# Kernel tuning notes

Hardware: AMD Instinct MI355X
Metric: run time of the kernel (lower is better)

Reference implementation:

```python
import jax, jax.numpy as jnp
import numpy as np

N = 50000      # nodes
E = 400000     # edges (avg degree 8)
N_IN = 256     # n_in_chan
N_HID = 256    # n_hid_chan


def gcn_conv(x, src, dst, W, b, n):
    """PyG GCNConv: D^{-1/2}(A+I)D^{-1/2} X W^T + b (add_self_loops=True, unit weights)."""
    h = x @ W.T                                           # [n, out]
    # degree over A + I: each node has a self loop (the initial ones) plus in-edges
    deg = jnp.ones((n,), h.dtype).at[dst].add(1.0)        # [n]
    dinv = jax.lax.rsqrt(deg)                             # deg >= 1 always
    norm = dinv[src] * dinv[dst]                          # [E]
    agg = jnp.zeros_like(h).at[dst].add(h[src] * norm[:, None])
    agg = agg + h * (dinv * dinv)[:, None]                # self-loop term, norm = dinv_i^2
    return agg + b


def setup_inputs() -> dict:
    key = jax.random.key(0)
    k1, k2, k3, k4 = jax.random.split(key, 4)
    x = jax.random.normal(k1, (N, N_IN + N_HID), dtype=jnp.float32)
    edge_index = jax.random.randint(k2, (2, E), 0, N, dtype=jnp.int64)
    s1 = 1.0 / np.sqrt(N_IN + N_HID)
    s2 = 1.0 / np.sqrt(N_HID)
    W1 = jax.random.normal(k3, (N_HID, N_IN + N_HID), dtype=jnp.float32) * s1
    W2 = jax.random.normal(k4, (N_HID, N_HID), dtype=jnp.float32) * s2
    b1 = jnp.zeros((N_HID,), jnp.float32)
    b2 = jnp.zeros((N_HID,), jnp.float32)
    return {"x": x, "edge_index": edge_index, "W1": W1, "b1": b1, "W2": W2, "b2": b2}


def reference(x, edge_index, W1, b1, W2, b2):
    src, dst = edge_index[0], edge_index[1]
    h = jax.nn.relu(gcn_conv(x, src, dst, W1, b1, N))
    return gcn_conv(h, src, dst, W2, b2, N)
```

## Files before the change

kernel.cpp:

```cpp
#include <hip/hip_runtime.h>
#include <hip/hip_bf16.h>

#define NN 50000
#define CH 256
#define SLOTS 96
#define G1K 512
#define G2K 256

typedef unsigned short u16;
typedef unsigned int   u32;

using short8 = __attribute__((ext_vector_type(8))) short;
using u16x8  = __attribute__((ext_vector_type(8))) unsigned short;
using f32x4  = __attribute__((ext_vector_type(4))) float;

static __device__ __forceinline__ float4 ld4(const float* p){ return *(const float4*)p; }

static __device__ __forceinline__ u16 f2b(float f){
  u32 u = __float_as_uint(f);
  u = (u + 0x7fffu + ((u >> 16) & 1u)) >> 16;
  return (u16)u;
}
static __device__ __forceinline__ float b2f(u16 b){
  return __uint_as_float(((u32)b) << 16);
}
static __device__ __forceinline__ int pkbf(float lo, float hi){
  __hip_bfloat162 h = __float22bfloat162_rn(make_float2(lo, hi));
  int r; __builtin_memcpy(&r, &h, 4); return r;
}

static __device__ __forceinline__ void gload_lds16(const void* g, void* l){
  __builtin_amdgcn_global_load_lds((const __attribute__((address_space(1))) void*)g,
                                   (__attribute__((address_space(3))) void*)l, 16, 0, 0);
}

#define WBAR(vm) do{ \
    asm volatile("s_waitcnt vmcnt(" #vm ") lgkmcnt(0)" ::: "memory"); \
    __builtin_amdgcn_s_barrier(); \
  }while(0)


__global__ void ell_build_kernel(const int* __restrict__ src, const int* __restrict__ dst,
                                 int* __restrict__ deg, int* __restrict__ ell, int E,
                                 const float* __restrict__ W1, u16* __restrict__ W1bf, int w1n4,
                                 const float* __restrict__ W2, u16* __restrict__ W2bf, int w2n4){
  int T = gridDim.x * 256;
  int g = blockIdx.x*256 + threadIdx.x;
  if (g < E){
    int d = dst[g];
    int pos = atomicAdd(&deg[d], 1);
    if (pos < SLOTS) ell[(size_t)d*SLOTS + pos] = src[g];
  }
  for (int i = g; i < w1n4; i += T){
    float4 v = ld4(W1 + (size_t)i*4);
    int2 o = { pkbf(v.x,v.y), pkbf(v.z,v.w) };
    *(int2*)(W1bf + (size_t)i*4) = o;
  }
  for (int i = g; i < w2n4; i += T){
    float4 v = ld4(W2 + (size_t)i*4);
    int2 o = { pkbf(v.x,v.y), pkbf(v.z,v.w) };
    *(int2*)(W2bf + (size_t)i*4) = o;
  }
}

__global__ void dinv_kernel(const int* __restrict__ deg, float* __restrict__ dinv, int n){
  int i = blockIdx.x*256 + threadIdx.x;
  if (i < n) dinv[i] = rsqrtf(1.0f + (float)deg[i]);
}


#define G1_GLB_B(kt, bb) do{ \
    gload_lds16(gB + (size_t)(kt)*32,          &Bs[bb][wave*2048]); \
    gload_lds16(gB + (size_t)(kt)*32 + 16*G1K, &Bs[bb][wave*2048 + 512]); \
    gload_lds16(gB + (size_t)(kt)*32 + 32*G1K, &Bs[bb][wave*2048 + 1024]); \
    gload_lds16(gB + (size_t)(kt)*32 + 48*G1K, &Bs[bb][wave*2048 + 1536]); \
  }while(0)

#define G1_GLB_A(kt, ab) do{ \
    gload_lds16(gA0 + (size_t)(kt)*32, &Asf[ab][wave*512]); \
    gload_lds16(gA1 + (size_t)(kt)*32, &Asf[ab][wave*512 + 256]); \
  }while(0)

#define G1_COMP(ra, rb) do{ \
    short8 af[4], bq[4]; \
    _Pragma("unroll") \
    for (int i=0;i<4;i++){ \
      int r = i*16 + lm; \
      float4 f0 = *(const float4*)&Asf[ra][r*32 + ((s0 ^ (lm&7))<<2)]; \
      float4 f1 = *(const float4*)&Asf[ra][r*32 + ((s1 ^ (lm&7))<<2)]; \
      int4 p = { pkbf(f0.x,f0.y), pkbf(f0.z,f0.w), pkbf(f1.x,f1.y), pkbf(f1.z,f1.w) }; \
      af[i] = *(short8*)&p; \
    } \
    _Pragma("unroll") \
    for (int j=0;j<4;j++) bq[j] = *(const short8*)&Bs[rb][(wave*64 + j*16 + lm)*32 + lk]; \
    _Pragma("unroll") \
    for (int i=0;i<4;i++) \
      _Pragma("unroll") \
      for (int j=0;j<4;j++) \
        acc[i][j] = __builtin_amdgcn_mfma_f32_16x16x32_bf16(af[i], bq[j], acc[i][j], 0, 0, 0); \
  }while(0)

__global__ __launch_bounds__(256, 2) void gemm1_kernel(const float* __restrict__ A,
                                                       const u16* __restrict__ Bbf,
                                                       u16* __restrict__ C, int M){
  __shared__ float Asf[3][64*32];
  __shared__ u16   Bs[2][256*32];
  int tid = threadIdx.x;
  int wave = tid >> 6, lane = tid & 63;
  int bm = blockIdx.x;

  int cslot = (lane & 7) ^ (lane >> 3);
  int r0 = bm*64 + wave*16 + (lane>>3);     if (r0 > M-1) r0 = M-1;
  int r1 = r0 + 8;                          if (r1 > M-1) r1 = M-1;
  const float* gA0 = A + (size_t)r0*G1K + cslot*4;
  const float* gA1 = A + (size_t)r1*G1K + cslot*4;
  const u16* gB = Bbf + (size_t)(wave*64 + (lane>>2))*G1K + (lane&3)*8;

  int lm = lane & 15;
  int lk = (lane >> 4) * 8;
  int s0 = (lane >> 4) * 2;
  int s1 = s0 + 1;

  f32x4 acc[4][4] = {};

  G1_GLB_B(0, 0);
  G1_GLB_A(0, 0);
  G1_GLB_A(1, 1);
  WBAR(2);

  G1_GLB_B( 1,1); G1_COMP(0,0); G1_GLB_A( 2,2); WBAR(2);
  G1_GLB_B( 2,0); G1_COMP(1,1); G1_GLB_A( 3,0); WBAR(2);
  G1_GLB_B( 3,1); G1_COMP(2,0); G1_GLB_A( 4,1); WBAR(2);
  G1_GLB_B( 4,0); G1_COMP(0,1); G1_GLB_A( 5,2); WBAR(2);
  G1_GLB_B( 5,1); G1_COMP(1,0); G1_GLB_A( 6,0); WBAR(2);
  G1_GLB_B( 6,0); G1_COMP(2,1); G1_GLB_A( 7,1); WBAR(2);
  G1_GLB_B( 7,1); G1_COMP(0,0); G1_GLB_A( 8,2); WBAR(2);
  G1_GLB_B( 8,0); G1_COMP(1,1); G1_GLB_A( 9,0); WBAR(2);
  G1_GLB_B( 9,1); G1_COMP(2,0); G1_GLB_A(10,1); WBAR(2);
  G1_GLB_B(10,0); G1_COMP(0,1); G1_GLB_A(11,2); WBAR(2);
  G1_GLB_B(11,1); G1_COMP(1,0); G1_GLB_A(12,0); WBAR(2);
  G1_GLB_B(12,0); G1_COMP(2,1); G1_GLB_A(13,1); WBAR(2);
  G1_GLB_B(13,1); G1_COMP(0,0); G1_GLB_A(14,2); WBAR(2);
  G1_GLB_B(14,0); G1_COMP(1,1); G1_GLB_A(15,0); WBAR(2);
  G1_GLB_B(15,1); G1_COMP(2,0);                 WBAR(0);
                  G1_COMP(0,1);

  int rb = (lane >> 4) * 4;
  #pragma unroll
  for (int i=0;i<4;i++){
    #pragma unroll
    for (int r=0;r<4;r++){
      int row = bm*64 + i*16 + rb + r;
      if (row < M){
        #pragma unroll
        for (int j=0;j<4;j++){
          int col = wave*64 + j*16 + lm;
          C[(size_t)row*CH + col] = f2b(acc[i][j][r]);
        }
      }
    }
  }
}


#define G2_GLB(kt, bb) do{ \
    gload_lds16(gA + (size_t)(kt)*32,          &As2[bb][wave*512]); \
    gload_lds16(gB + (size_t)(kt)*32,          &Bs2[bb][wave*2048]); \
    gload_lds16(gB + (size_t)(kt)*32 + 16*G2K, &Bs2[bb][wave*2048 + 512]); \
    gload_lds16(gB + (size_t)(kt)*32 + 32*G2K, &Bs2[bb][wave*2048 + 1024]); \
    gload_lds16(gB + (size_t)(kt)*32 + 48*G2K, &Bs2[bb][wave*2048 + 1536]); \
  }while(0)

#define G2_COMP(rb) do{ \
    short8 af[4], bq[4]; \
    _Pragma("unroll") \
    for (int i=0;i<4;i++) af[i] = *(const short8*)&As2[rb][(i*16 + lm)*32 + lk]; \
    _Pragma("unroll") \
    for (int j=0;j<4;j++) bq[j] = *(const short8*)&Bs2[rb][(wave*64 + j*16 + lm)*32 + lk]; \
    _Pragma("unroll") \
    for (int i=0;i<4;i++) \
      _Pragma("unroll") \
      for (int j=0;j<4;j++) \
        acc[i][j] = __builtin_amdgcn_mfma_f32_16x16x32_bf16(af[i], bq[j], acc[i][j], 0, 0, 0); \
  }while(0)

__global__ __launch_bounds__(256, 4) void gemm2_kernel(const u16* __restrict__ A,
                                                       const u16* __restrict__ B,
                                                       float* __restrict__ Cout,
                                                       const float* __restrict__ bias, int M){
  __shared__ u16 As2[3][64*32];
  __shared__ u16 Bs2[3][256*32];
  int tid = threadIdx.x;
  int wave = tid >> 6, lane = tid & 63;
  int bm = blockIdx.x;

  int ar = bm*64 + wave*16 + (lane>>2); if (ar > M-1) ar = M-1;
  const u16* gA = A + (size_t)ar*G2K + (lane&3)*8;
  const u16* gB = B + (size_t)(wave*64 + (lane>>2))*G2K + (lane&3)*8;

  int lm = lane & 15;
  int lk = (lane >> 4) * 8;

  f32x4 acc[4][4] = {};

  G2_GLB(0, 0);
  G2_GLB(1, 1);
  WBAR(5);

  G2_GLB(2,2); G2_COMP(0); WBAR(5);
  G2_GLB(3,0); G2_COMP(1); WBAR(5);
  G2_GLB(4,1); G2_COMP(2); WBAR(5);
  G2_GLB(5,2); G2_COMP(0); WBAR(5);
  G2_GLB(6,0); G2_COMP(1); WBAR(5);
  G2_GLB(7,1); G2_COMP(2); WBAR(5);
               G2_COMP(0); WBAR(0);
               G2_COMP(1);

  float bv[4];
  #pragma unroll
  for (int j=0;j<4;j++) bv[j] = bias[wave*64 + j*16 + lm];

  int rb = (lane >> 4) * 4;
  #pragma unroll
  for (int i=0;i<4;i++){
    #pragma unroll
    for (int r=0;r<4;r++){
      int row = bm*64 + i*16 + rb + r;
      if (row < M){
        #pragma unroll
        for (int j=0;j<4;j++){
          int col = wave*64 + j*16 + lm;
          Cout[(size_t)row*CH + col] = acc[i][j][r] + bv[j];
        }
      }
    }
  }
}


template<bool RELU, bool BIAS, bool OUTBF>
__global__ __launch_bounds__(256) void aggregate_kernel(const u16* __restrict__ h,
                                                        const float* __restrict__ bias,
                                                        const int* __restrict__ deg,
                                                        const float* __restrict__ dinv,
                                                        const int* __restrict__ ell,
                                                        void* __restrict__ outv, int n){
  int wave = threadIdx.x >> 6;
  int lane = threadIdx.x & 63;
  int i = blockIdx.x*4 + wave;
  if (i >= n) return;
  int half = lane >> 5;
  int c = (lane & 31) * 8;

  int degi = deg[i];
  float di = dinv[i];
  int m = degi < SLOTS ? degi : SLOTS;
  const int* row = ell + (size_t)i*SLOTS;

  float acc[8];
  #pragma unroll
  for (int k=0;k<8;k++) acc[k] = 0.f;

  int e = half;
  for (; e + 6 < m; e += 8){
    int s0 = row[e],   s1 = row[e+2], s2 = row[e+4], s3 = row[e+6];
    float n0 = dinv[s0] * di;
    float n1 = dinv[s1] * di;
    float n2 = dinv[s2] * di;
    float n3 = dinv[s3] * di;
    u16x8 h0 = *(const u16x8*)(h + (size_t)s0*CH + c);
    u16x8 h1 = *(const u16x8*)(h + (size_t)s1*CH + c);
    u16x8 h2 = *(const u16x8*)(h + (size_t)s2*CH + c);
    u16x8 h3 = *(const u16x8*)(h + (size_t)s3*CH + c);
    #pragma unroll
    for (int k=0;k<8;k++) acc[k] += b2f(h0[k])*n0;
    #pragma unroll
    for (int k=0;k<8;k++) acc[k] += b2f(h1[k])*n1;
    #pragma unroll
    for (int k=0;k<8;k++) acc[k] += b2f(h2[k])*n2;
    #pragma unroll
    for (int k=0;k<8;k++) acc[k] += b2f(h3[k])*n3;
  }
  for (; e < m; e += 2){
    int s0 = row[e];
    float n0 = dinv[s0] * di;
    u16x8 h0 = *(const u16x8*)(h + (size_t)s0*CH + c);
    #pragma unroll
    for (int k=0;k<8;k++) acc[k] += b2f(h0[k])*n0;
  }

  if (half == 0){
    float w = di*di;
    u16x8 hv = *(const u16x8*)(h + (size_t)i*CH + c);
    #pragma unroll
    for (int k=0;k<8;k++) acc[k] += b2f(hv[k])*w;
    if (BIAS){
      float4 b0 = ld4(bias + c), b1 = ld4(bias + c + 4);
      acc[0] += b0.x; acc[1] += b0.y; acc[2] += b0.z; acc[3] += b0.w;
      acc[4] += b1.x; acc[5] += b1.y; acc[6] += b1.z; acc[7] += b1.w;
    }
  }

  #pragma unroll
  for (int k=0;k<8;k++) acc[k] += __shfl_xor(acc[k], 32, 64);

  if (half == 0){
    if (RELU){
      #pragma unroll
      for (int k=0;k<8;k++) acc[k] = fmaxf(acc[k], 0.f);
    }
    if (OUTBF){
      u16x8 o;
      #pragma unroll
      for (int k=0;k<8;k++) o[k] = f2b(acc[k]);
      *(u16x8*)((u16*)outv + (size_t)i*CH + c) = o;
    } else {
      float* op = (float*)outv + (size_t)i*CH + c;
      *(float4*)op       = make_float4(acc[0],acc[1],acc[2],acc[3]);
      *(float4*)(op + 4) = make_float4(acc[4],acc[5],acc[6],acc[7]);
    }
  }
}


extern "C" void kernel_launch(void* const* d_in, const int* in_sizes, int n_in,
                              void* d_out, int out_size, void* d_ws, size_t ws_size,
                              hipStream_t stream){
  const float* x  = (const float*)d_in[0];
  const int*   ei = (const int*)d_in[1];
  const float* W1 = (const float*)d_in[2];
  const float* b1 = (const float*)d_in[3];
  const float* W2 = (const float*)d_in[4];
  const float* b2 = (const float*)d_in[5];
  float* out = (float*)d_out;

  const int n = NN;
  const int E = in_sizes[1] / 2;
  const int* src = ei;
  const int* dst = ei + E;

  char* ws = (char*)d_ws;
  size_t off = 0;
  auto alloc = [&](size_t bytes)->char* {
    char* p = ws + off;
    off += (bytes + 255) & ~(size_t)255;
    return p;
  };
  u16*   h1bf   = (u16*)  alloc((size_t)n*CH*sizeof(u16));
  u16*   h2bf   = (u16*)  alloc((size_t)n*CH*sizeof(u16));
  u16*   W1bf   = (u16*)  alloc((size_t)CH*G1K*sizeof(u16));
  u16*   W2bf   = (u16*)  alloc((size_t)CH*CH*sizeof(u16));
  int*   deg    = (int*)  alloc((size_t)n*sizeof(int));
  float* dinv   = (float*)alloc((size_t)n*sizeof(float));
  int*   ell    = (int*)  alloc((size_t)n*SLOTS*sizeof(int));
  (void)ws_size;

  u16* g1out = (u16*)d_out;

  hipMemsetAsync(deg, 0, (size_t)n*sizeof(int), stream);
  ell_build_kernel<<<(E+255)/256, 256, 0, stream>>>(src, dst, deg, ell, E,
                                                    W1, W1bf, CH*G1K/4,
                                                    W2, W2bf, CH*CH/4);
  dinv_kernel<<<(n+255)/256, 256, 0, stream>>>(deg, dinv, n);

  dim3 gg((n+63)/64);

  gemm1_kernel<<<gg, 256, 0, stream>>>(x, W1bf, g1out, n);
  aggregate_kernel<true, true, true><<<(n+3)/4, 256, 0, stream>>>(g1out, b1, deg, dinv, ell, h1bf, n);

  aggregate_kernel<false, false, true><<<(n+3)/4, 256, 0, stream>>>(h1bf, b2, deg, dinv, ell, h2bf, n);
  gemm2_kernel<<<gg, 256, 0, stream>>>(h2bf, W2bf, out, b2, n);
}
```

Before: 320.7 us.

## Fold source-side degree normalization into producers, drop dinv gathers and kernel

Prescales rows by the source-node rsqrt degree in the gemm1 epilogue and in the layer-1 aggregate output, so the aggregation loops become plain sums with no per-neighbor dinv gathers or multiplies. The destination-side factor is applied once at the end. This also removes the separate dinv kernel and buffer by computing rsqrt inline from deg. Prescaled values are stored in bf16, which slightly changes rounding.

New measurement: 319.9 us. About the same (-0.2%).

```diff
diff --git a/kernel.cpp b/kernel.cpp
--- a/kernel.cpp
+++ b/kernel.cpp
@@ -63,11 +63,6 @@
   }
 }
 
-__global__ void dinv_kernel(const int* __restrict__ deg, float* __restrict__ dinv, int n){
-  int i = blockIdx.x*256 + threadIdx.x;
-  if (i < n) dinv[i] = rsqrtf(1.0f + (float)deg[i]);
-}
-
 
 #define G1_GLB_B(kt, bb) do{ \
     gload_lds16(gB + (size_t)(kt)*32,          &Bs[bb][wave*2048]); \
@@ -102,6 +97,7 @@
 
 __global__ __launch_bounds__(256, 2) void gemm1_kernel(const float* __restrict__ A,
                                                        const u16* __restrict__ Bbf,
+                                                       const int* __restrict__ deg,
                                                        u16* __restrict__ C, int M){
   __shared__ float Asf[3][64*32];
   __shared__ u16   Bs[2][256*32];
@@ -152,10 +148,11 @@
     for (int r=0;r<4;r++){
       int row = bm*64 + i*16 + rb + r;
       if (row < M){
+        float dr = rsqrtf(1.0f + (float)deg[row]);
         #pragma unroll
         for (int j=0;j<4;j++){
           int col = wave*64 + j*16 + lm;
-          C[(size_t)row*CH + col] = f2b(acc[i][j][r]);
+          C[(size_t)row*CH + col] = f2b(acc[i][j][r] * dr);
         }
       }
     }
@@ -238,13 +235,12 @@
 }
 
 
-template<bool RELU, bool BIAS, bool OUTBF>
+template<bool RELU, bool BIAS, bool SCALEOUT>
 __global__ __launch_bounds__(256) void aggregate_kernel(const u16* __restrict__ h,
                                                         const float* __restrict__ bias,
                                                         const int* __restrict__ deg,
-                                                        const float* __restrict__ dinv,
                                                         const int* __restrict__ ell,
-                                                        void* __restrict__ outv, int n){
+                                                        u16* __restrict__ outv, int n){
   int wave = threadIdx.x >> 6;
   int lane = threadIdx.x & 63;
   int i = blockIdx.x*4 + wave;
@@ -253,7 +249,7 @@
   int c = (lane & 31) * 8;
 
   int degi = deg[i];
-  float di = dinv[i];
+  float di = rsqrtf(1.0f + (float)degi);
   int m = degi < SLOTS ? degi : SLOTS;
   const int* row = ell + (size_t)i*SLOTS;
 
@@ -263,62 +259,53 @@
 
   int e = half;
   for (; e + 6 < m; e += 8){
-    int s0 = row[e],   s1 = row[e+2], s2 = row[e+4], s3 = row[e+6];
-    float n0 = dinv[s0] * di;
-    float n1 = dinv[s1] * di;
-    float n2 = dinv[s2] * di;
-    float n3 = dinv[s3] * di;
+    int s0 = row[e], s1 = row[e+2], s2 = row[e+4], s3 = row[e+6];
     u16x8 h0 = *(const u16x8*)(h + (size_t)s0*CH + c);
     u16x8 h1 = *(const u16x8*)(h + (size_t)s1*CH + c);
     u16x8 h2 = *(const u16x8*)(h + (size_t)s2*CH + c);
     u16x8 h3 = *(const u16x8*)(h + (size_t)s3*CH + c);
     #pragma unroll
-    for (int k=0;k<8;k++) acc[k] += b2f(h0[k])*n0;
-    #pragma unroll
-    for (int k=0;k<8;k++) acc[k] += b2f(h1[k])*n1;
-    #pragma unroll
-    for (int k=0;k<8;k++) acc[k] += b2f(h2[k])*n2;
-    #pragma unroll
-    for (int k=0;k<8;k++) acc[k] += b2f(h3[k])*n3;
+    for (int k=0;k<8;k++) acc[k] += b2f(h0[k]);
+    #pragma unroll
+    for (int k=0;k<8;k++) acc[k] += b2f(h1[k]);
+    #pragma unroll
+    for (int k=0;k<8;k++) acc[k] += b2f(h2[k]);
+    #pragma unroll
+    for (int k=0;k<8;k++) acc[k] += b2f(h3[k]);
   }
   for (; e < m; e += 2){
     int s0 = row[e];
-    float n0 = dinv[s0] * di;
     u16x8 h0 = *(const u16x8*)(h + (size_t)s0*CH + c);
     #pragma unroll
-    for (int k=0;k<8;k++) acc[k] += b2f(h0[k])*n0;
+    for (int k=0;k<8;k++) acc[k] += b2f(h0[k]);
   }
 
   if (half == 0){
-    float w = di*di;
     u16x8 hv = *(const u16x8*)(h + (size_t)i*CH + c);
     #pragma unroll
-    for (int k=0;k<8;k++) acc[k] += b2f(hv[k])*w;
+    for (int k=0;k<8;k++) acc[k] += b2f(hv[k]);
+  }
+
+  #pragma unroll
+  for (int k=0;k<8;k++) acc[k] += __shfl_xor(acc[k], 32, 64);
+
+  if (half == 0){
+    float bv[8];
     if (BIAS){
       float4 b0 = ld4(bias + c), b1 = ld4(bias + c + 4);
-      acc[0] += b0.x; acc[1] += b0.y; acc[2] += b0.z; acc[3] += b0.w;
-      acc[4] += b1.x; acc[5] += b1.y; acc[6] += b1.z; acc[7] += b1.w;
+      bv[0]=b0.x; bv[1]=b0.y; bv[2]=b0.z; bv[3]=b0.w;
+      bv[4]=b1.x; bv[5]=b1.y; bv[6]=b1.z; bv[7]=b1.w;
     }
-  }
-
-  #pragma unroll
-  for (int k=0;k<8;k++) acc[k] += __shfl_xor(acc[k], 32, 64);
-
-  if (half == 0){
-    if (RELU){
-      #pragma unroll
-      for (int k=0;k<8;k++) acc[k] = fmaxf(acc[k], 0.f);
+    u16x8 o;
+    #pragma unroll
+    for (int k=0;k<8;k++){
+      float v = acc[k] * di;
+      if (BIAS) v += bv[k];
+      if (RELU) v = fmaxf(v, 0.f);
+      if (SCALEOUT) v *= di;
+      o[k] = f2b(v);
     }
-    if (OUTBF){
-      u16x8 o;
-      #pragma unroll
-      for (int k=0;k<8;k++) o[k] = f2b(acc[k]);
-      *(u16x8*)((u16*)outv + (size_t)i*CH + c) = o;
-    } else {
-      float* op = (float*)outv + (size_t)i*CH + c;
-      *(float4*)op       = make_float4(acc[0],acc[1],acc[2],acc[3]);
-      *(float4*)(op + 4) = make_float4(acc[4],acc[5],acc[6],acc[7]);
-    }
+    *(u16x8*)(outv + (size_t)i*CH + c) = o;
   }
 }
 
@@ -351,7 +338,6 @@
   u16*   W1bf   = (u16*)  alloc((size_t)CH*G1K*sizeof(u16));
   u16*   W2bf   = (u16*)  alloc((size_t)CH*CH*sizeof(u16));
   int*   deg    = (int*)  alloc((size_t)n*sizeof(int));
-  float* dinv   = (float*)alloc((size_t)n*sizeof(float));
   int*   ell    = (int*)  alloc((size_t)n*SLOTS*sizeof(int));
   (void)ws_size;
 
@@ -361,13 +347,12 @@
   ell_build_kernel<<<(E+255)/256, 256, 0, stream>>>(src, dst, deg, ell, E,
                                                     W1, W1bf, CH*G1K/4,
                                                     W2, W2bf, CH*CH/4);
-  dinv_kernel<<<(n+255)/256, 256, 0, stream>>>(deg, dinv, n);
 
   dim3 gg((n+63)/64);
 
-  gemm1_kernel<<<gg, 256, 0, stream>>>(x, W1bf, g1out, n);
-  aggregate_kernel<true, true, true><<<(n+3)/4, 256, 0, stream>>>(g1out, b1, deg, dinv, ell, h1bf, n);
-
-  aggregate_kernel<false, false, true><<<(n+3)/4, 256, 0, stream>>>(h1bf, b2, deg, dinv, ell, h2bf, n);
+  gemm1_kernel<<<gg, 256, 0, stream>>>(x, W1bf, deg, g1out, n);
+  aggregate_kernel<true, true, true><<<(n+3)/4, 256, 0, stream>>>(g1out, b1, deg, ell, h1bf, n);
+
+  aggregate_kernel<false, false, false><<<(n+3)/4, 256, 0, stream>>>(h1bf, b2, deg, ell, h2bf, n);
   gemm2_kernel<<<gg, 256, 0, stream>>>(h2bf, W2bf, out, b2, n);
 }
```
